# Optimization experiments

Hardware: AMD Instinct MI355X
Metric: run time of the kernel (lower is better)

Reference implementation:

```python
import jax, jax.numpy as jnp
import numpy as np

D_MODEL = 1024
N_HEADS = 16
D_HEAD = D_MODEL // N_HEADS
D_FF = 4096
EPS = 1e-5


def layer_norm(x, g, b):
    mu = jnp.mean(x, axis=-1, keepdims=True)
    var = jnp.mean(jnp.square(x - mu), axis=-1, keepdims=True)
    return (x - mu) * jax.lax.rsqrt(var + EPS) * g + b


def setup_inputs() -> dict:
    key = jax.random.key(0)
    ks = jax.random.split(key, 8)
    s = 1.0 / np.sqrt(D_MODEL)
    return {
        "x": jax.random.normal(ks[0], (2, 2048, D_MODEL), dtype=jnp.float32),
        "Wq": jax.random.normal(ks[1], (N_HEADS, D_MODEL, D_HEAD), dtype=jnp.float32) * s,
        "Wk": jax.random.normal(ks[2], (N_HEADS, D_MODEL, D_HEAD), dtype=jnp.float32) * s,
        "Wv": jax.random.normal(ks[3], (N_HEADS, D_MODEL, D_HEAD), dtype=jnp.float32) * s,
        "Wo": jax.random.normal(ks[4], (D_MODEL, D_MODEL), dtype=jnp.float32) * s,
        "bo": jnp.zeros((D_MODEL,), dtype=jnp.float32),
        "ln1_g": jnp.ones((D_MODEL,), dtype=jnp.float32),
        "ln1_b": jnp.zeros((D_MODEL,), dtype=jnp.float32),
        "ln2_g": jnp.ones((D_MODEL,), dtype=jnp.float32),
        "ln2_b": jnp.zeros((D_MODEL,), dtype=jnp.float32),
        "W1": jax.random.normal(ks[5], (D_MODEL, D_FF), dtype=jnp.float32) * s,
        "b1": jnp.zeros((D_FF,), dtype=jnp.float32),
        "W2": jax.random.normal(ks[6], (D_FF, D_MODEL), dtype=jnp.float32) * (1.0 / np.sqrt(D_FF)),
        "b2": jnp.zeros((D_MODEL,), dtype=jnp.float32),
    }


def reference(x, Wq, Wk, Wv, Wo, bo, ln1_g, ln1_b, ln2_g, ln2_b, W1, b1, W2, b2):
    # Pre-norm MHA (per-head projections batched over head axis h)
    xn = layer_norm(x, ln1_g, ln1_b)
    q = jnp.einsum("bsd,hde->bhse", xn, Wq)
    k = jnp.einsum("bsd,hde->bhse", xn, Wk)
    v = jnp.einsum("bsd,hde->bhse", xn, Wv)
    scores = jnp.einsum("bhqe,bhke->bhqk", q, k) / jnp.sqrt(jnp.float32(D_HEAD))
    w = jax.nn.softmax(scores, axis=-1)
    attn = jnp.einsum("bhqk,bhke->bhqe", w, v)  # [b,h,s,dh]
    b, h, s, dh = attn.shape
    concat = attn.transpose(0, 2, 1, 3).reshape(b, s, h * dh)  # head concat order matches torch cat
    attn_out = concat @ Wo + bo
    hidden = x + attn_out
    hn = layer_norm(hidden, ln2_g, ln2_b)
    ff = jax.nn.gelu(hn @ W1 + b1, approximate=False) @ W2 + b2  # torch nn.GELU default = exact
    return hidden + ff
```

## Files before the change

kernel.cpp:

```cpp
#include <hip/hip_runtime.h>
#include <hip/hip_bf16.h>

typedef __bf16 bf16;
typedef __bf16 bf16x8 __attribute__((ext_vector_type(8)));
typedef float  f32x4  __attribute__((ext_vector_type(4)));

static __device__ __forceinline__ f32x4 mfma16(bf16x8 a, bf16x8 b, f32x4 c) {
  return __builtin_amdgcn_mfma_f32_16x16x32_bf16(a, b, c, 0, 0, 0);
}

static __device__ __forceinline__ void gl_lds16(const bf16* g, bf16* l) {
  __builtin_amdgcn_global_load_lds(
      (const __attribute__((address_space(1))) void*)g,
      (__attribute__((address_space(3))) void*)l, 16, 0, 0);
}

template <bool IN_F32>
__global__ __launch_bounds__(256) void tr_kernel(const void* __restrict__ inp,
                                                 bf16* __restrict__ out,
                                                 int R, int C) {
  __shared__ bf16 tile[32][33];
  const size_t zoff = (size_t)blockIdx.z * R * C;
  const int tx = threadIdx.x & 31, ty = threadIdx.x >> 5;
  const int x = blockIdx.x * 32 + tx;
  const int y0 = blockIdx.y * 32;
#pragma unroll
  for (int j = 0; j < 4; ++j) {
    const size_t i = zoff + (size_t)(y0 + ty + j * 8) * C + x;
    tile[ty + j * 8][tx] =
        IN_F32 ? (bf16)((const float*)inp)[i] : ((const bf16*)inp)[i];
  }
  __syncthreads();
  const int x2 = y0 + tx;
  const int y2 = blockIdx.x * 32;
#pragma unroll
  for (int j = 0; j < 4; ++j)
    out[zoff + (size_t)(y2 + ty + j * 8) * R + x2] = tile[tx][ty + j * 8];
}

__global__ __launch_bounds__(256) void ln_kernel(const float* __restrict__ inp,
                                                 const float* __restrict__ g,
                                                 const float* __restrict__ bt,
                                                 bf16* __restrict__ outp) {
  const int row = blockIdx.x;
  const int t = threadIdx.x;
  f32x4 v = ((const f32x4*)inp)[row * 256 + t];
  float s = v[0] + v[1] + v[2] + v[3];
  float sq = v[0] * v[0] + v[1] * v[1] + v[2] * v[2] + v[3] * v[3];
#pragma unroll
  for (int off = 32; off > 0; off >>= 1) {
    s += __shfl_xor(s, off);
    sq += __shfl_xor(sq, off);
  }
  __shared__ float red[8];
  const int wave = t >> 6, lane = t & 63;
  if (lane == 0) {
    red[wave] = s;
    red[wave + 4] = sq;
  }
  __syncthreads();
  s = red[0] + red[1] + red[2] + red[3];
  sq = red[4] + red[5] + red[6] + red[7];
  const float mu = s * (1.0f / 1024.0f);
  const float var = sq * (1.0f / 1024.0f) - mu * mu;
  const float rstd = rsqrtf(fmaxf(var, 0.0f) + 1e-5f);
  f32x4 gg = ((const f32x4*)g)[t];
  f32x4 bb = ((const f32x4*)bt)[t];
  bf16 o[4];
#pragma unroll
  for (int i = 0; i < 4; ++i)
    o[i] = (bf16)((v[i] - mu) * rstd * gg[i] + bb[i]);
  *(uint2*)&outp[(size_t)row * 1024 + 4 * t] = *(uint2*)o;
}

enum { EPI_QKV = 0, EPI_O = 1, EPI_FF1 = 2, EPI_FF2 = 3 };

template <int EPI>
__global__ __launch_bounds__(256) void gemm_bt(
    const bf16* __restrict__ A, const bf16* __restrict__ Bt, const int K,
    const float* __restrict__ bias, const float* __restrict__ res,
    bf16* __restrict__ outB, float* __restrict__ outF) {
  __shared__ __align__(16) bf16 sA[128 * 64];
  __shared__ __align__(16) bf16 sB[128 * 64];
  const int t = threadIdx.x;
  const int lane = t & 63, wave = t >> 6;
  const int quad = lane >> 4, l15 = lane & 15;
  const int wr = wave >> 1, wc = wave & 1;
  const int m0 = blockIdx.y * 128, n0 = blockIdx.x * 128;
  const int srow = lane >> 3;
  const int scol = ((lane & 7) ^ srow) * 8;

  f32x4 acc[4][4];
#pragma unroll
  for (int i = 0; i < 4; ++i)
#pragma unroll
    for (int j = 0; j < 4; ++j) acc[i][j] = {0.f, 0.f, 0.f, 0.f};

  for (int kt = 0; kt < K; kt += 64) {
    __syncthreads();
#pragma unroll
    for (int c = 0; c < 4; ++c) {
      const int chunk = wave * 4 + c;
      const int row = chunk * 8 + srow;
      gl_lds16(&A[(size_t)(m0 + row) * K + kt + scol], &sA[chunk * 512]);
      gl_lds16(&Bt[(size_t)(n0 + row) * K + kt + scol], &sB[chunk * 512]);
    }
    __syncthreads();
#pragma unroll
    for (int ks = 0; ks < 2; ++ks) {
      bf16x8 af[4], bfr[4];
#pragma unroll
      for (int mi = 0; mi < 4; ++mi) {
        const int row = wr * 64 + mi * 16 + l15;
        const int col = ((ks * 4 + quad) ^ (row & 7)) * 8;
        af[mi] = *(const bf16x8*)&sA[row * 64 + col];
      }
#pragma unroll
      for (int ni = 0; ni < 4; ++ni) {
        const int row = wc * 64 + ni * 16 + l15;
        const int col = ((ks * 4 + quad) ^ (row & 7)) * 8;
        bfr[ni] = *(const bf16x8*)&sB[row * 64 + col];
      }
#pragma unroll
      for (int mi = 0; mi < 4; ++mi)
#pragma unroll
        for (int ni = 0; ni < 4; ++ni)
          acc[mi][ni] = mfma16(af[mi], bfr[ni], acc[mi][ni]);
    }
  }

#pragma unroll
  for (int mi = 0; mi < 4; ++mi) {
#pragma unroll
    for (int ni = 0; ni < 4; ++ni) {
      const int n = n0 + wc * 64 + ni * 16 + l15;
#pragma unroll
      for (int r = 0; r < 4; ++r) {
        const int m = m0 + wr * 64 + mi * 16 + quad * 4 + r;
        float v = acc[mi][ni][r];
        if constexpr (EPI == EPI_QKV) {
          const int which = n >> 10, nn = n & 1023;
          const int h = nn >> 6, e = nn & 63;
          const int b = m >> 11, s2 = m & 2047;
          outB[(size_t)which * 4194304 +
               ((size_t)(b * 16 + h) * 2048 + s2) * 64 + e] = (bf16)v;
        } else if constexpr (EPI == EPI_O) {
          v += bias[n] + res[(size_t)m * 1024 + n];
          outF[(size_t)m * 1024 + n] = v;
        } else if constexpr (EPI == EPI_FF1) {
          v += bias[n];
          v = 0.5f * v * (1.0f + erff(v * 0.70710678118654752f));
          outB[(size_t)m * 4096 + n] = (bf16)v;
        } else {
          v += bias[n] + res[(size_t)m * 1024 + n];
          outF[(size_t)m * 1024 + n] = v;
        }
      }
    }
  }
}

__global__ __launch_bounds__(256) void attn_kernel(const bf16* __restrict__ q,
                                                   const bf16* __restrict__ k,
                                                   const bf16* __restrict__ vt,
                                                   bf16* __restrict__ ao) {
  __shared__ __align__(16) bf16 sQ[128 * 64];
  __shared__ __align__(16) bf16 sK[64 * 64];
  __shared__ __align__(16) bf16 sV[64 * 64];
  __shared__ __align__(16) bf16 sP[128 * 72];
  const int t = threadIdx.x;
  const int lane = t & 63, wave = t >> 6;
  const int quad = lane >> 4, l15 = lane & 15;
  const int q0 = blockIdx.x * 128;
  const int bh = blockIdx.y;
  const int b = bh >> 4, h = bh & 15;
  const bf16* Q = q + (size_t)bh * 2048 * 64;
  const bf16* Kp = k + (size_t)bh * 2048 * 64;
  const bf16* Vt = vt + (size_t)bh * 64 * 2048;
  const int srow = lane >> 3;
  const int scol = ((lane & 7) ^ srow) * 8;
  const float SCL = 0.125f * 1.4426950408889634f;

#pragma unroll
  for (int c = 0; c < 4; ++c) {
    const int chunk = wave * 4 + c;
    const int row = chunk * 8 + srow;
    gl_lds16(&Q[(size_t)(q0 + row) * 64 + scol], &sQ[chunk * 512]);
  }
  __syncthreads();
  bf16x8 qf[2][2];
#pragma unroll
  for (int mi = 0; mi < 2; ++mi)
#pragma unroll
    for (int ks = 0; ks < 2; ++ks) {
      const int row = wave * 32 + mi * 16 + l15;
      const int col = ((ks * 4 + quad) ^ (row & 7)) * 8;
      qf[mi][ks] = *(const bf16x8*)&sQ[row * 64 + col];
    }

  f32x4 o[2][4];
  float lsum[2][4];
#pragma unroll
  for (int mi = 0; mi < 2; ++mi) {
#pragma unroll
    for (int ne = 0; ne < 4; ++ne) o[mi][ne] = {0.f, 0.f, 0.f, 0.f};
#pragma unroll
    for (int r = 0; r < 4; ++r) lsum[mi][r] = 0.f;
  }

  for (int kb = 0; kb < 32; ++kb) {
    const int kbase = kb * 64;
    __syncthreads();
    {
#pragma unroll
      for (int c = 0; c < 2; ++c) {
        const int chunk = wave * 2 + c;
        const int row = chunk * 8 + srow;
        gl_lds16(&Kp[(size_t)(kbase + row) * 64 + scol], &sK[chunk * 512]);
        gl_lds16(&Vt[(size_t)row * 2048 + kbase + scol], &sV[chunk * 512]);
      }
    }
    __syncthreads();

    f32x4 s[2][4];
#pragma unroll
    for (int mi = 0; mi < 2; ++mi)
#pragma unroll
      for (int ni = 0; ni < 4; ++ni) s[mi][ni] = {0.f, 0.f, 0.f, 0.f};
#pragma unroll
    for (int ks = 0; ks < 2; ++ks) {
      bf16x8 kf[4];
#pragma unroll
      for (int ni = 0; ni < 4; ++ni) {
        const int row = ni * 16 + l15;
        const int col = ((ks * 4 + quad) ^ (row & 7)) * 8;
        kf[ni] = *(const bf16x8*)&sK[row * 64 + col];
      }
#pragma unroll
      for (int mi = 0; mi < 2; ++mi)
#pragma unroll
        for (int ni = 0; ni < 4; ++ni)
          s[mi][ni] = mfma16(qf[mi][ks], kf[ni], s[mi][ni]);
    }

#pragma unroll
    for (int mi = 0; mi < 2; ++mi)
#pragma unroll
      for (int ni = 0; ni < 4; ++ni)
#pragma unroll
        for (int r = 0; r < 4; ++r) {
          const float p = exp2f(s[mi][ni][r] * SCL);
          lsum[mi][r] += p;
          sP[(wave * 32 + mi * 16 + quad * 4 + r) * 72 + ni * 16 + l15] =
              (bf16)p;
        }

#pragma unroll
    for (int ksb = 0; ksb < 2; ++ksb) {
      bf16x8 pf[2], vf[4];
#pragma unroll
      for (int mi = 0; mi < 2; ++mi)
        pf[mi] = *(const bf16x8*)&sP[(wave * 32 + mi * 16 + l15) * 72 +
                                     ksb * 32 + quad * 8];
#pragma unroll
      for (int ne = 0; ne < 4; ++ne) {
        const int row = ne * 16 + l15;
        const int col = ((ksb * 4 + quad) ^ (row & 7)) * 8;
        vf[ne] = *(const bf16x8*)&sV[row * 64 + col];
      }
#pragma unroll
      for (int mi = 0; mi < 2; ++mi)
#pragma unroll
        for (int ne = 0; ne < 4; ++ne)
          o[mi][ne] = mfma16(pf[mi], vf[ne], o[mi][ne]);
    }
  }

#pragma unroll
  for (int mi = 0; mi < 2; ++mi)
#pragma unroll
    for (int r = 0; r < 4; ++r) {
      float xs = lsum[mi][r];
      xs += __shfl_xor(xs, 1);
      xs += __shfl_xor(xs, 2);
      xs += __shfl_xor(xs, 4);
      xs += __shfl_xor(xs, 8);
      lsum[mi][r] = 1.0f / fmaxf(xs, 1e-30f);
    }
#pragma unroll
  for (int mi = 0; mi < 2; ++mi)
#pragma unroll
    for (int ne = 0; ne < 4; ++ne)
#pragma unroll
      for (int r = 0; r < 4; ++r) {
        const int row = q0 + wave * 32 + mi * 16 + quad * 4 + r;
        const int col = h * 64 + ne * 16 + l15;
        ao[((size_t)(b * 2048 + row)) * 1024 + col] =
            (bf16)(o[mi][ne][r] * lsum[mi][r]);
      }
}

extern "C" void kernel_launch(void* const* d_in, const int* in_sizes, int n_in,
                              void* d_out, int out_size, void* d_ws,
                              size_t ws_size, hipStream_t stream) {
  const float* x    = (const float*)d_in[0];
  const float* Wq   = (const float*)d_in[1];
  const float* Wk   = (const float*)d_in[2];
  const float* Wv   = (const float*)d_in[3];
  const float* Wo   = (const float*)d_in[4];
  const float* bo   = (const float*)d_in[5];
  const float* ln1g = (const float*)d_in[6];
  const float* ln1b = (const float*)d_in[7];
  const float* ln2g = (const float*)d_in[8];
  const float* ln2b = (const float*)d_in[9];
  const float* W1   = (const float*)d_in[10];
  const float* b1   = (const float*)d_in[11];
  const float* W2   = (const float*)d_in[12];
  const float* b2   = (const float*)d_in[13];

  char* ws = (char*)d_ws;
  const size_t MB = 1ull << 20;
  bf16* QKVT = (bf16*)(ws);
  bf16* WqT  = QKVT;
  bf16* WkT  = (bf16*)(ws + 2 * MB);
  bf16* WvT  = (bf16*)(ws + 4 * MB);
  bf16* WoT  = (bf16*)(ws + 6 * MB);
  bf16* W1T  = (bf16*)(ws + 8 * MB);
  bf16* W2T  = (bf16*)(ws + 16 * MB);
  bf16* sh8  = (bf16*)(ws + 24 * MB);
  bf16* qb   = (bf16*)(ws + 32 * MB);
  bf16* kb   = (bf16*)(ws + 40 * MB);
  bf16* vb   = (bf16*)(ws + 48 * MB);
  bf16* vtb  = (bf16*)(ws + 56 * MB);
  bf16* h1   = (bf16*)(ws + 32 * MB);
  float* hid = (float*)(ws + 64 * MB);

  const dim3 blk(256);
  tr_kernel<true><<<dim3(2, 32, 16), blk, 0, stream>>>(Wq, WqT, 1024, 64);
  tr_kernel<true><<<dim3(2, 32, 16), blk, 0, stream>>>(Wk, WkT, 1024, 64);
  tr_kernel<true><<<dim3(2, 32, 16), blk, 0, stream>>>(Wv, WvT, 1024, 64);
  tr_kernel<true><<<dim3(32, 32, 1), blk, 0, stream>>>(Wo, WoT, 1024, 1024);
  tr_kernel<true><<<dim3(128, 32, 1), blk, 0, stream>>>(W1, W1T, 1024, 4096);
  tr_kernel<true><<<dim3(32, 128, 1), blk, 0, stream>>>(W2, W2T, 4096, 1024);

  ln_kernel<<<4096, blk, 0, stream>>>(x, ln1g, ln1b, sh8);
  gemm_bt<EPI_QKV><<<dim3(24, 32), blk, 0, stream>>>(
      sh8, QKVT, 1024, nullptr, nullptr, qb, nullptr);
  tr_kernel<false><<<dim3(2, 64, 32), blk, 0, stream>>>(vb, vtb, 2048, 64);
  attn_kernel<<<dim3(16, 32), blk, 0, stream>>>(qb, kb, vtb, sh8);
  gemm_bt<EPI_O><<<dim3(8, 32), blk, 0, stream>>>(
      sh8, WoT, 1024, bo, x, nullptr, hid);
  ln_kernel<<<4096, blk, 0, stream>>>(hid, ln2g, ln2b, sh8);
  gemm_bt<EPI_FF1><<<dim3(32, 32), blk, 0, stream>>>(
      sh8, W1T, 1024, b1, nullptr, h1, nullptr);
  gemm_bt<EPI_FF2><<<dim3(8, 32), blk, 0, stream>>>(
      h1, W2T, 4096, b2, hid, nullptr, (float*)d_out);

  (void)in_sizes; (void)n_in; (void)out_size; (void)ws_size;
}
```

Baseline: 412.8 us.

## Merge weight transposes, halve attention query tile, use narrow GEMM tiles for N=1024

The six weight-transpose launches become one table-driven kernel. The attention kernel now uses 64-query blocks with one 16-row tile per wave, computing S transposed so P can be written as bf16x4 vectors into a shared Q/P buffer. The O-projection and FF2 GEMMs switch to 128x64 tiles, which doubles their grid. The aim is to cut launch overhead and to fill more compute units on the small-grid kernels, at the cost of less data reuse per block.

Result: faster. 378.2 us (-8.4%).

```diff
diff --git a/kernel.cpp b/kernel.cpp
--- a/kernel.cpp
+++ b/kernel.cpp
@@ -2,6 +2,7 @@
 #include <hip/hip_bf16.h>
 
 typedef __bf16 bf16;
+typedef __bf16 bf16x4 __attribute__((ext_vector_type(4)));
 typedef __bf16 bf16x8 __attribute__((ext_vector_type(8)));
 typedef float  f32x4  __attribute__((ext_vector_type(4)));
 
@@ -15,21 +16,54 @@
       (__attribute__((address_space(3))) void*)l, 16, 0, 0);
 }
 
-template <bool IN_F32>
-__global__ __launch_bounds__(256) void tr_kernel(const void* __restrict__ inp,
-                                                 bf16* __restrict__ out,
-                                                 int R, int C) {
+struct TrTab {
+  const float* src[6];
+  bf16* dst[6];
+  int R[6], C[6], ntx[6], nty[6];
+  int base[7];
+};
+
+__global__ __launch_bounds__(256) void tr6_kernel(TrTab tab) {
+  int bid = blockIdx.x;
+  int j = 0;
+  while (j < 5 && bid >= tab.base[j + 1]) ++j;
+  const int local = bid - tab.base[j];
+  const int R = tab.R[j], C = tab.C[j];
+  const int ntx = tab.ntx[j];
+  const int per_z = ntx * tab.nty[j];
+  const int z = local / per_z;
+  const int rem = local - z * per_z;
+  const int by = rem / ntx, bx = rem - by * ntx;
+  const float* in = tab.src[j];
+  bf16* out = tab.dst[j];
+
+  __shared__ bf16 tile[32][33];
+  const size_t zoff = (size_t)z * R * C;
+  const int tx = threadIdx.x & 31, ty = threadIdx.x >> 5;
+  const int x = bx * 32 + tx;
+  const int y0 = by * 32;
+#pragma unroll
+  for (int jj = 0; jj < 4; ++jj)
+    tile[ty + jj * 8][tx] = (bf16)in[zoff + (size_t)(y0 + ty + jj * 8) * C + x];
+  __syncthreads();
+  const int x2 = y0 + tx;
+  const int y2 = bx * 32;
+#pragma unroll
+  for (int jj = 0; jj < 4; ++jj)
+    out[zoff + (size_t)(y2 + ty + jj * 8) * R + x2] = tile[tx][ty + jj * 8];
+}
+
+__global__ __launch_bounds__(256) void trb_kernel(const bf16* __restrict__ inp,
+                                                  bf16* __restrict__ out,
+                                                  int R, int C) {
   __shared__ bf16 tile[32][33];
   const size_t zoff = (size_t)blockIdx.z * R * C;
   const int tx = threadIdx.x & 31, ty = threadIdx.x >> 5;
   const int x = blockIdx.x * 32 + tx;
   const int y0 = blockIdx.y * 32;
 #pragma unroll
-  for (int j = 0; j < 4; ++j) {
-    const size_t i = zoff + (size_t)(y0 + ty + j * 8) * C + x;
-    tile[ty + j * 8][tx] =
-        IN_F32 ? (bf16)((const float*)inp)[i] : ((const bf16*)inp)[i];
-  }
+  for (int j = 0; j < 4; ++j)
+    tile[ty + j * 8][tx] = inp[zoff + (size_t)(y0 + ty + j * 8) * C + x];
   __syncthreads();
   const int x2 = y0 + tx;
   const int y2 = blockIdx.x * 32;
@@ -75,26 +109,28 @@
 
 enum { EPI_QKV = 0, EPI_O = 1, EPI_FF1 = 2, EPI_FF2 = 3 };
 
-template <int EPI>
+template <int EPI, bool NARROW>
 __global__ __launch_bounds__(256) void gemm_bt(
     const bf16* __restrict__ A, const bf16* __restrict__ Bt, const int K,
     const float* __restrict__ bias, const float* __restrict__ res,
     bf16* __restrict__ outB, float* __restrict__ outF) {
+  constexpr int BN = NARROW ? 64 : 128;
+  constexpr int NI = NARROW ? 2 : 4;
   __shared__ __align__(16) bf16 sA[128 * 64];
-  __shared__ __align__(16) bf16 sB[128 * 64];
+  __shared__ __align__(16) bf16 sB[BN * 64];
   const int t = threadIdx.x;
   const int lane = t & 63, wave = t >> 6;
   const int quad = lane >> 4, l15 = lane & 15;
   const int wr = wave >> 1, wc = wave & 1;
-  const int m0 = blockIdx.y * 128, n0 = blockIdx.x * 128;
+  const int m0 = blockIdx.y * 128, n0 = blockIdx.x * BN;
   const int srow = lane >> 3;
   const int scol = ((lane & 7) ^ srow) * 8;
 
-  f32x4 acc[4][4];
+  f32x4 acc[4][NI];
 #pragma unroll
   for (int i = 0; i < 4; ++i)
 #pragma unroll
-    for (int j = 0; j < 4; ++j) acc[i][j] = {0.f, 0.f, 0.f, 0.f};
+    for (int j = 0; j < NI; ++j) acc[i][j] = {0.f, 0.f, 0.f, 0.f};
 
   for (int kt = 0; kt < K; kt += 64) {
     __syncthreads();
@@ -103,12 +139,17 @@
       const int chunk = wave * 4 + c;
       const int row = chunk * 8 + srow;
       gl_lds16(&A[(size_t)(m0 + row) * K + kt + scol], &sA[chunk * 512]);
+    }
+#pragma unroll
+    for (int c = 0; c < BN / 32; ++c) {
+      const int chunk = wave * (BN / 32) + c;
+      const int row = chunk * 8 + srow;
       gl_lds16(&Bt[(size_t)(n0 + row) * K + kt + scol], &sB[chunk * 512]);
     }
     __syncthreads();
 #pragma unroll
     for (int ks = 0; ks < 2; ++ks) {
-      bf16x8 af[4], bfr[4];
+      bf16x8 af[4], bfr[NI];
 #pragma unroll
       for (int mi = 0; mi < 4; ++mi) {
         const int row = wr * 64 + mi * 16 + l15;
@@ -116,15 +157,15 @@
         af[mi] = *(const bf16x8*)&sA[row * 64 + col];
       }
 #pragma unroll
-      for (int ni = 0; ni < 4; ++ni) {
-        const int row = wc * 64 + ni * 16 + l15;
+      for (int ni = 0; ni < NI; ++ni) {
+        const int row = wc * (BN / 2) + ni * 16 + l15;
         const int col = ((ks * 4 + quad) ^ (row & 7)) * 8;
         bfr[ni] = *(const bf16x8*)&sB[row * 64 + col];
       }
 #pragma unroll
       for (int mi = 0; mi < 4; ++mi)
 #pragma unroll
-        for (int ni = 0; ni < 4; ++ni)
+        for (int ni = 0; ni < NI; ++ni)
           acc[mi][ni] = mfma16(af[mi], bfr[ni], acc[mi][ni]);
     }
   }
@@ -132,8 +173,8 @@
 #pragma unroll
   for (int mi = 0; mi < 4; ++mi) {
 #pragma unroll
-    for (int ni = 0; ni < 4; ++ni) {
-      const int n = n0 + wc * 64 + ni * 16 + l15;
+    for (int ni = 0; ni < NI; ++ni) {
+      const int n = n0 + wc * (BN / 2) + ni * 16 + l15;
 #pragma unroll
       for (int r = 0; r < 4; ++r) {
         const int m = m0 + wr * 64 + mi * 16 + quad * 4 + r;
@@ -164,14 +205,13 @@
                                                    const bf16* __restrict__ k,
                                                    const bf16* __restrict__ vt,
                                                    bf16* __restrict__ ao) {
-  __shared__ __align__(16) bf16 sQ[128 * 64];
+  __shared__ __align__(16) bf16 sQP[64 * 72];
   __shared__ __align__(16) bf16 sK[64 * 64];
   __shared__ __align__(16) bf16 sV[64 * 64];
-  __shared__ __align__(16) bf16 sP[128 * 72];
   const int t = threadIdx.x;
   const int lane = t & 63, wave = t >> 6;
   const int quad = lane >> 4, l15 = lane & 15;
-  const int q0 = blockIdx.x * 128;
+  const int q0 = blockIdx.x * 64;
   const int bh = blockIdx.y;
   const int b = bh >> 4, h = bh & 15;
   const bf16* Q = q + (size_t)bh * 2048 * 64;
@@ -182,51 +222,40 @@
   const float SCL = 0.125f * 1.4426950408889634f;
 
 #pragma unroll
-  for (int c = 0; c < 4; ++c) {
-    const int chunk = wave * 4 + c;
+  for (int c = 0; c < 2; ++c) {
+    const int chunk = wave * 2 + c;
     const int row = chunk * 8 + srow;
-    gl_lds16(&Q[(size_t)(q0 + row) * 64 + scol], &sQ[chunk * 512]);
+    gl_lds16(&Q[(size_t)(q0 + row) * 64 + scol], &sQP[chunk * 512]);
   }
   __syncthreads();
-  bf16x8 qf[2][2];
-#pragma unroll
-  for (int mi = 0; mi < 2; ++mi)
-#pragma unroll
-    for (int ks = 0; ks < 2; ++ks) {
-      const int row = wave * 32 + mi * 16 + l15;
-      const int col = ((ks * 4 + quad) ^ (row & 7)) * 8;
-      qf[mi][ks] = *(const bf16x8*)&sQ[row * 64 + col];
-    }
-
-  f32x4 o[2][4];
-  float lsum[2][4];
-#pragma unroll
-  for (int mi = 0; mi < 2; ++mi) {
-#pragma unroll
-    for (int ne = 0; ne < 4; ++ne) o[mi][ne] = {0.f, 0.f, 0.f, 0.f};
-#pragma unroll
-    for (int r = 0; r < 4; ++r) lsum[mi][r] = 0.f;
-  }
+  bf16x8 qf[2];
+#pragma unroll
+  for (int ks = 0; ks < 2; ++ks) {
+    const int row = wave * 16 + l15;
+    const int col = ((ks * 4 + quad) ^ (row & 7)) * 8;
+    qf[ks] = *(const bf16x8*)&sQP[row * 64 + col];
+  }
+
+  f32x4 o[4];
+  float lsum = 0.f;
+#pragma unroll
+  for (int ne = 0; ne < 4; ++ne) o[ne] = {0.f, 0.f, 0.f, 0.f};
 
   for (int kb = 0; kb < 32; ++kb) {
     const int kbase = kb * 64;
     __syncthreads();
-    {
-#pragma unroll
-      for (int c = 0; c < 2; ++c) {
-        const int chunk = wave * 2 + c;
-        const int row = chunk * 8 + srow;
-        gl_lds16(&Kp[(size_t)(kbase + row) * 64 + scol], &sK[chunk * 512]);
-        gl_lds16(&Vt[(size_t)row * 2048 + kbase + scol], &sV[chunk * 512]);
-      }
+#pragma unroll
+    for (int c = 0; c < 2; ++c) {
+      const int chunk = wave * 2 + c;
+      const int row = chunk * 8 + srow;
+      gl_lds16(&Kp[(size_t)(kbase + row) * 64 + scol], &sK[chunk * 512]);
+      gl_lds16(&Vt[(size_t)row * 2048 + kbase + scol], &sV[chunk * 512]);
     }
     __syncthreads();
 
-    f32x4 s[2][4];
-#pragma unroll
-    for (int mi = 0; mi < 2; ++mi)
-#pragma unroll
-      for (int ni = 0; ni < 4; ++ni) s[mi][ni] = {0.f, 0.f, 0.f, 0.f};
+    f32x4 s[4];
+#pragma unroll
+    for (int ni = 0; ni < 4; ++ni) s[ni] = {0.f, 0.f, 0.f, 0.f};
 #pragma unroll
     for (int ks = 0; ks < 2; ++ks) {
       bf16x8 kf[4];
@@ -237,31 +266,27 @@
         kf[ni] = *(const bf16x8*)&sK[row * 64 + col];
       }
 #pragma unroll
-      for (int mi = 0; mi < 2; ++mi)
-#pragma unroll
-        for (int ni = 0; ni < 4; ++ni)
-          s[mi][ni] = mfma16(qf[mi][ks], kf[ni], s[mi][ni]);
-    }
-
-#pragma unroll
-    for (int mi = 0; mi < 2; ++mi)
-#pragma unroll
       for (int ni = 0; ni < 4; ++ni)
-#pragma unroll
-        for (int r = 0; r < 4; ++r) {
-          const float p = exp2f(s[mi][ni][r] * SCL);
-          lsum[mi][r] += p;
-          sP[(wave * 32 + mi * 16 + quad * 4 + r) * 72 + ni * 16 + l15] =
-              (bf16)p;
-        }
+        s[ni] = mfma16(kf[ni], qf[ks], s[ni]);
+    }
+
+#pragma unroll
+    for (int ni = 0; ni < 4; ++ni) {
+      bf16x4 p4;
+#pragma unroll
+      for (int r = 0; r < 4; ++r) {
+        const float p = exp2f(s[ni][r] * SCL);
+        lsum += p;
+        p4[r] = (bf16)p;
+      }
+      *(bf16x4*)&sQP[(wave * 16 + l15) * 72 + ni * 16 + quad * 4] = p4;
+    }
 
 #pragma unroll
     for (int ksb = 0; ksb < 2; ++ksb) {
-      bf16x8 pf[2], vf[4];
-#pragma unroll
-      for (int mi = 0; mi < 2; ++mi)
-        pf[mi] = *(const bf16x8*)&sP[(wave * 32 + mi * 16 + l15) * 72 +
-                                     ksb * 32 + quad * 8];
+      bf16x8 pf = *(const bf16x8*)&sQP[(wave * 16 + l15) * 72 +
+                                       ksb * 32 + quad * 8];
+      bf16x8 vf[4];
 #pragma unroll
       for (int ne = 0; ne < 4; ++ne) {
         const int row = ne * 16 + l15;
@@ -269,35 +294,27 @@
         vf[ne] = *(const bf16x8*)&sV[row * 64 + col];
       }
 #pragma unroll
-      for (int mi = 0; mi < 2; ++mi)
-#pragma unroll
-        for (int ne = 0; ne < 4; ++ne)
-          o[mi][ne] = mfma16(pf[mi], vf[ne], o[mi][ne]);
-    }
-  }
-
-#pragma unroll
-  for (int mi = 0; mi < 2; ++mi)
+      for (int ne = 0; ne < 4; ++ne)
+        o[ne] = mfma16(pf, vf[ne], o[ne]);
+    }
+  }
+
+  lsum += __shfl_xor(lsum, 16);
+  lsum += __shfl_xor(lsum, 32);
+  const float linv_q = 1.0f / fmaxf(lsum, 1e-30f);
+  float linv[4];
+#pragma unroll
+  for (int r = 0; r < 4; ++r)
+    linv[r] = __shfl(linv_q, quad * 4 + r);
+#pragma unroll
+  for (int ne = 0; ne < 4; ++ne)
 #pragma unroll
     for (int r = 0; r < 4; ++r) {
-      float xs = lsum[mi][r];
-      xs += __shfl_xor(xs, 1);
-      xs += __shfl_xor(xs, 2);
-      xs += __shfl_xor(xs, 4);
-      xs += __shfl_xor(xs, 8);
-      lsum[mi][r] = 1.0f / fmaxf(xs, 1e-30f);
-    }
-#pragma unroll
-  for (int mi = 0; mi < 2; ++mi)
-#pragma unroll
-    for (int ne = 0; ne < 4; ++ne)
-#pragma unroll
-      for (int r = 0; r < 4; ++r) {
-        const int row = q0 + wave * 32 + mi * 16 + quad * 4 + r;
-        const int col = h * 64 + ne * 16 + l15;
-        ao[((size_t)(b * 2048 + row)) * 1024 + col] =
-            (bf16)(o[mi][ne][r] * lsum[mi][r]);
-      }
+      const int row = q0 + wave * 16 + quad * 4 + r;
+      const int col = h * 64 + ne * 16 + l15;
+      ao[((size_t)(b * 2048 + row)) * 1024 + col] =
+          (bf16)(o[ne][r] * linv[r]);
+    }
 }
 
 extern "C" void kernel_launch(void* const* d_in, const int* in_sizes, int n_in,
@@ -336,24 +353,38 @@
   float* hid = (float*)(ws + 64 * MB);
 
   const dim3 blk(256);
-  tr_kernel<true><<<dim3(2, 32, 16), blk, 0, stream>>>(Wq, WqT, 1024, 64);
-  tr_kernel<true><<<dim3(2, 32, 16), blk, 0, stream>>>(Wk, WkT, 1024, 64);
-  tr_kernel<true><<<dim3(2, 32, 16), blk, 0, stream>>>(Wv, WvT, 1024, 64);
-  tr_kernel<true><<<dim3(32, 32, 1), blk, 0, stream>>>(Wo, WoT, 1024, 1024);
-  tr_kernel<true><<<dim3(128, 32, 1), blk, 0, stream>>>(W1, W1T, 1024, 4096);
-  tr_kernel<true><<<dim3(32, 128, 1), blk, 0, stream>>>(W2, W2T, 4096, 1024);
+
+  TrTab tab;
+  const float* srcs[6] = {Wq, Wk, Wv, Wo, W1, W2};
+  bf16* dsts[6] = {WqT, WkT, WvT, WoT, W1T, W2T};
+  const int Rs[6] = {1024, 1024, 1024, 1024, 1024, 4096};
+  const int Cs[6] = {64, 64, 64, 1024, 4096, 1024};
+  const int Zs[6] = {16, 16, 16, 1, 1, 1};
+  int base = 0;
+  for (int j = 0; j < 6; ++j) {
+    tab.src[j] = srcs[j];
+    tab.dst[j] = dsts[j];
+    tab.R[j] = Rs[j];
+    tab.C[j] = Cs[j];
+    tab.ntx[j] = Cs[j] / 32;
+    tab.nty[j] = Rs[j] / 32;
+    tab.base[j] = base;
+    base += (Cs[j] / 32) * (Rs[j] / 32) * Zs[j];
+  }
+  tab.base[6] = base;
+  tr6_kernel<<<base, blk, 0, stream>>>(tab);
 
   ln_kernel<<<4096, blk, 0, stream>>>(x, ln1g, ln1b, sh8);
-  gemm_bt<EPI_QKV><<<dim3(24, 32), blk, 0, stream>>>(
+  gemm_bt<EPI_QKV, false><<<dim3(24, 32), blk, 0, stream>>>(
       sh8, QKVT, 1024, nullptr, nullptr, qb, nullptr);
-  tr_kernel<false><<<dim3(2, 64, 32), blk, 0, stream>>>(vb, vtb, 2048, 64);
-  attn_kernel<<<dim3(16, 32), blk, 0, stream>>>(qb, kb, vtb, sh8);
-  gemm_bt<EPI_O><<<dim3(8, 32), blk, 0, stream>>>(
+  trb_kernel<<<dim3(2, 64, 32), blk, 0, stream>>>(vb, vtb, 2048, 64);
+  attn_kernel<<<dim3(32, 32), blk, 0, stream>>>(qb, kb, vtb, sh8);
+  gemm_bt<EPI_O, true><<<dim3(16, 32), blk, 0, stream>>>(
       sh8, WoT, 1024, bo, x, nullptr, hid);
   ln_kernel<<<4096, blk, 0, stream>>>(hid, ln2g, ln2b, sh8);
-  gemm_bt<EPI_FF1><<<dim3(32, 32), blk, 0, stream>>>(
+  gemm_bt<EPI_FF1, false><<<dim3(32, 32), blk, 0, stream>>>(
       sh8, W1T, 1024, b1, nullptr, h1, nullptr);
-  gemm_bt<EPI_FF2><<<dim3(8, 32), blk, 0, stream>>>(
+  gemm_bt<EPI_FF2, true><<<dim3(16, 32), blk, 0, stream>>>(
       h1, W2T, 4096, b2, hid, nullptr, (float*)d_out);
 
   (void)in_sizes; (void)n_in; (void)out_size; (void)ws_size;
```
